# Optimization experiments

Measured on AMD Instinct MI355X. Metric: run time of the kernel, lower is better.

## Reference

```python
import jax, jax.numpy as jnp
import numpy as np

B, E, V, L = 16384, 16, 1_000_000, 50
DENSE, ONEHOT, MULTIHOT = 13, 26, 2
UNITS = [64, 12]
NN_IN = E * (ONEHOT + MULTIHOT) + DENSE  # 16*28+13 = 461
CONCAT_IN = 1 + E + UNITS[-1]            # 29


def setup_inputs() -> dict:
    key = jax.random.key(0)
    ks = jax.random.split(key, 12)
    s = 0.02  # glorot-ish init scale
    return {
        "dense": jax.random.normal(ks[0], (B, DENSE), jnp.float32),
        "onehot": jax.random.randint(ks[1], (B, ONEHOT), 0, V, jnp.int32),
        "multihot_ids": jax.random.randint(ks[2], (B, MULTIHOT, L), 0, V, jnp.int32),
        "multihot_mask": jnp.ones((B, MULTIHOT, L), jnp.float32),
        "fm_w": jax.random.normal(ks[3], (V, 1), jnp.float32) * s,
        "fm_emb": jax.random.normal(ks[4], (V, E), jnp.float32) * s,
        "nn_w0": jax.random.normal(ks[5], (NN_IN, UNITS[0]), jnp.float32) * s,
        "nn_b0": jnp.zeros((UNITS[0],), jnp.float32),
        "nn_w1": jax.random.normal(ks[6], (UNITS[0], UNITS[1]), jnp.float32) * s,
        "nn_b1": jnp.zeros((UNITS[1],), jnp.float32),
        "concat_w": jax.random.normal(ks[7], (CONCAT_IN, 1), jnp.float32) * s,
        "concat_b": jnp.zeros((1,), jnp.float32),
    }


def reference(dense, onehot, multihot_ids, multihot_mask, fm_w, fm_emb,
              nn_w0, nn_b0, nn_w1, nn_b1, concat_w, concat_b):
    # --- embedding lookups ---
    onehot_emb = fm_emb[onehot]                      # [B, 26, E]
    mh_emb = fm_emb[multihot_ids]                    # [B, 2, L, E]
    m = multihot_mask[..., None]                     # [B, 2, L, 1]
    # embedding_lookup_sparse(combiner='mean') over valid slots; empty rows -> 0 (tf.pad)
    denom = jnp.maximum(jnp.sum(m, axis=2), 1.0)     # [B, 2, 1]
    multihot_emb = jnp.sum(mh_emb * m, axis=2) / denom  # [B, 2, E]
    cat_emb = jnp.concatenate([onehot_emb, multihot_emb], axis=1)  # [B, 28, E]

    # --- FM 1st order: sum_i w_i (x_i = 1) ---
    fm_1st = jnp.sum(fm_w[onehot], axis=1)           # [B, 1]

    # --- FM 2nd order (keep_k_dims=True): 0.5*((sum v)^2 - sum v^2) ---
    s = jnp.sum(cat_emb, axis=1)                     # [B, E]
    fm_2nd = 0.5 * (s * s - jnp.sum(cat_emb * cat_emb, axis=1))  # [B, E]

    # --- deep part ---
    nn_inp = jnp.concatenate([cat_emb.reshape(-1, E * (ONEHOT + MULTIHOT)), dense], axis=1)
    h = jax.nn.relu(nn_inp @ nn_w0 + nn_b0)
    h = jax.nn.relu(h @ nn_w1 + nn_b1)               # [B, 12]

    concat_inp = jnp.concatenate([fm_1st, fm_2nd, h], axis=1)  # [B, 29]
    return jax.nn.sigmoid(concat_inp @ concat_w + concat_b)    # [B, 1]
```

## Files before the change

kernel.cpp:

```cpp
#include <hip/hip_runtime.h>
#include <hip/hip_bf16.h>

#define BATCH 16384
#define EDIM  16
#define NOH   26
#define LL    50
#define KIN   461
#define KPAD  480
#define KLDS  488
#define ROWS  32

using bf16x8 = __attribute__((ext_vector_type(8))) short;
using f32x4  = __attribute__((ext_vector_type(4))) float;

static __device__ __forceinline__ unsigned short f2bf(float f) {
    union { float f; unsigned int u; } v; v.f = f;
    unsigned int r = v.u + 0x7FFFu + ((v.u >> 16) & 1u);
    return (unsigned short)(r >> 16);
}
static __device__ __forceinline__ float bf2f(unsigned short u) {
    union { unsigned int u; float f; } v; v.u = ((unsigned int)u) << 16;
    return v.f;
}

__global__ __launch_bounds__(256) void prep(const float* __restrict__ w0,
                                            unsigned short* __restrict__ w0f) {
    int idx = blockIdx.x * 256 + threadIdx.x;
    if (idx < 30720) {
        int j    = idx & 7;
        int frag = idx >> 3;
        int lane = frag & 63;
        int tile = frag >> 6;
        int nt = tile / 15;
        int kt = tile - nt * 15;
        int k = kt * 32 + ((lane >> 4) << 3) + j;
        int n = (nt << 4) + (lane & 15);
        float v = (k < KIN) ? w0[k * 64 + n] : 0.f;
        w0f[idx] = f2bf(v);
    }
}

__global__ __launch_bounds__(512, 4) void fused(
    const float* __restrict__ dense,
    const int*   __restrict__ onehot,
    const int*   __restrict__ mh_ids,
    const float* __restrict__ mh_mask,
    const float* __restrict__ fm_w,
    const float* __restrict__ fm_emb,
    const unsigned short* __restrict__ w0f,
    const float* __restrict__ b0,
    const float* __restrict__ w1,
    const float* __restrict__ b1,
    const float* __restrict__ concat_w,
    const float* __restrict__ concat_b,
    float* __restrict__ out)
{
    __shared__ unsigned short As[ROWS * KLDS];
    __shared__ unsigned short h0s[ROWS][68];
    __shared__ float w1t[12 * 64];
    __shared__ float part_s[ROWS];
    __shared__ float b0s[64];
    __shared__ float b1s[12];
    __shared__ float cwh[12];

    const int t  = threadIdx.x;
    const int wv = t >> 6;
    const int l  = t & 63;
    const int s  = l >> 2;
    const int d  = l & 3;
    const int row0 = blockIdx.x << 5;

    for (int i = t; i < 768; i += 512) { int k = i / 12, j = i - k * 12; w1t[j * 64 + k] = w1[i]; }
    if (t < 64)               b0s[t] = b0[t];
    if (t >= 64 && t < 76)    b1s[t - 64] = b1[t - 64];
    if (t >= 96 && t < 108)   cwh[t - 96] = concat_w[17 + (t - 96)];

    for (int i = 0; i < 4; ++i) {
        const int r = (wv << 2) + i;
        const int b = row0 + r;

        const float v1 = (s < 10) ? 1.f : 0.f;
        int oid0 = onehot[b * NOH + s];
        int oid1 = (s < 10) ? onehot[b * NOH + 16 + s] : 0;

        int   mid[7]; float mmk[7];
        #pragma unroll
        for (int p = 0; p < 7; ++p) {
            int pi = p * 16 + s;
            bool valid = pi < 100;
            int f = (pi >= 50) ? 1 : 0;
            int ii = pi - f * 50;
            size_t off = ((size_t)b * 2 + f) * LL + ii;
            mid[p] = valid ? mh_ids[off]  : 0;
            mmk[p] = valid ? mh_mask[off] : 0.f;
        }

        float4 e0 = *(const float4*)(fm_emb + (size_t)oid0 * EDIM + d * 4);
        float4 e1 = *(const float4*)(fm_emb + (size_t)oid1 * EDIM + d * 4);
        float  wsa = fm_w[oid0];
        float  wsb = fm_w[oid1];
        float4 gm[7];
        #pragma unroll
        for (int p = 0; p < 7; ++p)
            gm[p] = *(const float4*)(fm_emb + (size_t)mid[p] * EDIM + d * 4);

        e1.x *= v1; e1.y *= v1; e1.z *= v1; e1.w *= v1;
        float wsum = (d == 0) ? (wsa + v1 * wsb) : 0.f;

        unsigned short* rowp = As + r * KLDS;
        {
            ushort4 u; u.x = f2bf(e0.x); u.y = f2bf(e0.y); u.z = f2bf(e0.z); u.w = f2bf(e0.w);
            *(ushort4*)(rowp + s * EDIM + d * 4) = u;
        }
        if (s < 10) {
            ushort4 u; u.x = f2bf(e1.x); u.y = f2bf(e1.y); u.z = f2bf(e1.z); u.w = f2bf(e1.w);
            *(ushort4*)(rowp + (16 + s) * EDIM + d * 4) = u;
        }

        float a0x=0,a0y=0,a0z=0,a0w=0, a1x=0,a1y=0,a1z=0,a1w=0, m0=0, m1=0;
        #pragma unroll
        for (int p = 0; p < 7; ++p) {
            int pi = p * 16 + s;
            float m = mmk[p];
            if (pi >= 50) { a1x += m*gm[p].x; a1y += m*gm[p].y; a1z += m*gm[p].z; a1w += m*gm[p].w; m1 += m; }
            else          { a0x += m*gm[p].x; a0y += m*gm[p].y; a0z += m*gm[p].z; a0w += m*gm[p].w; m0 += m; }
        }

        float ohx = e0.x + e1.x, ohy = e0.y + e1.y, ohz = e0.z + e1.z, ohw = e0.w + e1.w;
        float qx = e0.x*e0.x + e1.x*e1.x, qy = e0.y*e0.y + e1.y*e1.y;
        float qz = e0.z*e0.z + e1.z*e1.z, qw = e0.w*e0.w + e1.w*e1.w;

#define R4(v) { v += __shfl_xor(v, 4); v += __shfl_xor(v, 8); v += __shfl_xor(v, 16); v += __shfl_xor(v, 32); }
        R4(a0x) R4(a0y) R4(a0z) R4(a0w)
        R4(a1x) R4(a1y) R4(a1z) R4(a1w)
        R4(m0)  R4(m1)
        R4(ohx) R4(ohy) R4(ohz) R4(ohw)
        R4(qx)  R4(qy)  R4(qz)  R4(qw)
        R4(wsum)
#undef R4

        float inv0 = 1.f / fmaxf(m0, 1.f);
        float inv1 = 1.f / fmaxf(m1, 1.f);
        float h0x = a0x*inv0, h0y = a0y*inv0, h0z = a0z*inv0, h0w = a0w*inv0;
        float h1x = a1x*inv1, h1y = a1y*inv1, h1z = a1z*inv1, h1w = a1w*inv1;

        if (s == 0) {
            ushort4 u; u.x = f2bf(h0x); u.y = f2bf(h0y); u.z = f2bf(h0z); u.w = f2bf(h0w);
            *(ushort4*)(rowp + 26 * EDIM + d * 4) = u;
        }
        if (s == 1) {
            ushort4 u; u.x = f2bf(h1x); u.y = f2bf(h1y); u.z = f2bf(h1z); u.w = f2bf(h1w);
            *(ushort4*)(rowp + 27 * EDIM + d * 4) = u;
        }

        float sx = ohx + h0x + h1x, sy = ohy + h0y + h1y, sz = ohz + h0z + h1z, sw = ohw + h0w + h1w;
        float tx = qx + h0x*h0x + h1x*h1x, ty = qy + h0y*h0y + h1y*h1y;
        float tz = qz + h0z*h0z + h1z*h1z, tw = qw + h0w*h0w + h1w*h1w;
        float f2x = 0.5f * (sx*sx - tx), f2y = 0.5f * (sy*sy - ty);
        float f2z = 0.5f * (sz*sz - tz), f2w = 0.5f * (sw*sw - tw);

        float cw0 = concat_w[0];
        float c0 = concat_w[1 + d*4 + 0], c1 = concat_w[1 + d*4 + 1];
        float c2 = concat_w[1 + d*4 + 2], c3 = concat_w[1 + d*4 + 3];
        float part = f2x*c0 + f2y*c1 + f2z*c2 + f2w*c3 + wsum * cw0;
        part += __shfl_xor(part, 1);
        part += __shfl_xor(part, 2);
        if (l == 0) part_s[r] = part + concat_b[0];

        if (l < 32) {
            float v = (l < 13) ? dense[b * 13 + l] : 0.f;
            rowp[448 + l] = f2bf(v);
        }
    }
    __syncthreads();

    const int rt = wv >> 2, nt = wv & 3;
    const int c = l & 15, g = l >> 4;

    f32x4 acc = {0.f, 0.f, 0.f, 0.f};
    const unsigned short* ap = As + (rt * 16 + c) * KLDS + (g << 3);
    const unsigned short* bgp = w0f + ((size_t)(nt * 15) * 64 + l) * 8;

    #pragma unroll
    for (int kt = 0; kt < 15; ++kt) {
        bf16x8 a = *(const bf16x8*)(ap + kt * 32);
        bf16x8 bb = *(const bf16x8*)(bgp + (size_t)kt * 64 * 8);
        acc = __builtin_amdgcn_mfma_f32_16x16x32_bf16(a, bb, acc, 0, 0, 0);
    }

    #pragma unroll
    for (int reg = 0; reg < 4; ++reg)
        h0s[rt * 16 + g * 4 + reg][nt * 16 + c] = f2bf(fmaxf(acc[reg] + b0s[nt * 16 + c], 0.f));
    __syncthreads();

    if (wv < 2) {
        float s0 = b1s[g*3 + 0], s1 = b1s[g*3 + 1], s2 = b1s[g*3 + 2];
        const unsigned short* hrow = &h0s[wv * 16 + c][0];
        #pragma unroll
        for (int k8 = 0; k8 < 8; ++k8) {
            ushort4 ha = *(const ushort4*)(hrow + k8 * 8 + 0);
            ushort4 hb = *(const ushort4*)(hrow + k8 * 8 + 4);
            float h[8] = { bf2f(ha.x), bf2f(ha.y), bf2f(ha.z), bf2f(ha.w),
                           bf2f(hb.x), bf2f(hb.y), bf2f(hb.z), bf2f(hb.w) };
            #pragma unroll
            for (int j = 0; j < 8; ++j) {
                int k = k8 * 8 + j;
                s0 += h[j] * w1t[(g*3 + 0) * 64 + k];
                s1 += h[j] * w1t[(g*3 + 1) * 64 + k];
                s2 += h[j] * w1t[(g*3 + 2) * 64 + k];
            }
        }
        float hd = fmaxf(s0, 0.f)*cwh[g*3] + fmaxf(s1, 0.f)*cwh[g*3+1] + fmaxf(s2, 0.f)*cwh[g*3+2];
        hd += __shfl_xor(hd, 16);
        hd += __shfl_xor(hd, 32);
        if (g == 0) {
            int rr = row0 + wv * 16 + c;
            float x = part_s[wv * 16 + c] + hd;
            out[rr] = 1.f / (1.f + __expf(-x));
        }
    }
}

extern "C" void kernel_launch(void* const* d_in, const int* in_sizes, int n_in,
                              void* d_out, int out_size, void* d_ws, size_t ws_size,
                              hipStream_t stream) {
    const float* dense   = (const float*)d_in[0];
    const int*   onehot  = (const int*)  d_in[1];
    const int*   mh_ids  = (const int*)  d_in[2];
    const float* mh_mask = (const float*)d_in[3];
    const float* fm_w    = (const float*)d_in[4];
    const float* fm_emb  = (const float*)d_in[5];
    const float* w0      = (const float*)d_in[6];
    const float* b0      = (const float*)d_in[7];
    const float* w1      = (const float*)d_in[8];
    const float* b1      = (const float*)d_in[9];
    const float* cw      = (const float*)d_in[10];
    const float* cb      = (const float*)d_in[11];

    unsigned short* w0f = (unsigned short*)d_ws;

    hipLaunchKernelGGL(prep, dim3(120), dim3(256), 0, stream, w0, w0f);
    hipLaunchKernelGGL(fused, dim3(BATCH / ROWS), dim3(512), 0, stream,
                       dense, onehot, mh_ids, mh_mask, fm_w, fm_emb,
                       w0f, b0, w1, b1, cw, cb, (float*)d_out);
}
```

Baseline: 159.1 us.

## Overlap second-half embedding gather with first-half MFMA GEMM via warp specialization

The block's 32 rows are split into two 16-row halves. All 8 waves gather the first 16 rows. Then waves 0-3 run the MFMA layer-0 GEMM on that half while waves 4-7 gather the remaining 16 rows. The layer-1 tail for the first half overlaps with the second-half GEMM. The intent is to hide gather memory latency behind matrix work, at the cost of unbalanced per-wave work and an extra barrier stage.

```diff
diff --git a/kernel.cpp b/kernel.cpp
--- a/kernel.cpp
+++ b/kernel.cpp
@@ -75,10 +75,8 @@
     if (t >= 64 && t < 76)    b1s[t - 64] = b1[t - 64];
     if (t >= 96 && t < 108)   cwh[t - 96] = concat_w[17 + (t - 96)];
 
-    for (int i = 0; i < 4; ++i) {
-        const int r = (wv << 2) + i;
+    auto gather_row = [&](int r) {
         const int b = row0 + r;
-
         const float v1 = (s < 10) ? 1.f : 0.f;
         int oid0 = onehot[b * NOH + s];
         int oid1 = (s < 10) ? onehot[b * NOH + 16 + s] : 0;
@@ -171,54 +169,75 @@
             float v = (l < 13) ? dense[b * 13 + l] : 0.f;
             rowp[448 + l] = f2bf(v);
         }
-    }
-    __syncthreads();
-
-    const int rt = wv >> 2, nt = wv & 3;
+    };
+
     const int c = l & 15, g = l >> 4;
 
-    f32x4 acc = {0.f, 0.f, 0.f, 0.f};
-    const unsigned short* ap = As + (rt * 16 + c) * KLDS + (g << 3);
-    const unsigned short* bgp = w0f + ((size_t)(nt * 15) * 64 + l) * 8;
-
-    #pragma unroll
-    for (int kt = 0; kt < 15; ++kt) {
-        bf16x8 a = *(const bf16x8*)(ap + kt * 32);
-        bf16x8 bb = *(const bf16x8*)(bgp + (size_t)kt * 64 * 8);
-        acc = __builtin_amdgcn_mfma_f32_16x16x32_bf16(a, bb, acc, 0, 0, 0);
-    }
-
-    #pragma unroll
-    for (int reg = 0; reg < 4; ++reg)
-        h0s[rt * 16 + g * 4 + reg][nt * 16 + c] = f2bf(fmaxf(acc[reg] + b0s[nt * 16 + c], 0.f));
-    __syncthreads();
-
-    if (wv < 2) {
+    auto gemm_half = [&](int h, int nt) {
+        f32x4 acc = {0.f, 0.f, 0.f, 0.f};
+        const unsigned short* ap = As + (h * 16 + c) * KLDS + (g << 3);
+        const unsigned short* bgp = w0f + ((size_t)(nt * 15) * 64 + l) * 8;
+        #pragma unroll
+        for (int kt = 0; kt < 15; ++kt) {
+            bf16x8 a = *(const bf16x8*)(ap + kt * 32);
+            bf16x8 bb = *(const bf16x8*)(bgp + (size_t)kt * 64 * 8);
+            acc = __builtin_amdgcn_mfma_f32_16x16x32_bf16(a, bb, acc, 0, 0, 0);
+        }
+        #pragma unroll
+        for (int reg = 0; reg < 4; ++reg)
+            h0s[h * 16 + g * 4 + reg][nt * 16 + c] = f2bf(fmaxf(acc[reg] + b0s[nt * 16 + c], 0.f));
+    };
+
+    auto tail_half = [&](int h) {
         float s0 = b1s[g*3 + 0], s1 = b1s[g*3 + 1], s2 = b1s[g*3 + 2];
-        const unsigned short* hrow = &h0s[wv * 16 + c][0];
+        const unsigned short* hrow = &h0s[h * 16 + c][0];
         #pragma unroll
         for (int k8 = 0; k8 < 8; ++k8) {
             ushort4 ha = *(const ushort4*)(hrow + k8 * 8 + 0);
             ushort4 hb = *(const ushort4*)(hrow + k8 * 8 + 4);
-            float h[8] = { bf2f(ha.x), bf2f(ha.y), bf2f(ha.z), bf2f(ha.w),
-                           bf2f(hb.x), bf2f(hb.y), bf2f(hb.z), bf2f(hb.w) };
+            float hv[8] = { bf2f(ha.x), bf2f(ha.y), bf2f(ha.z), bf2f(ha.w),
+                            bf2f(hb.x), bf2f(hb.y), bf2f(hb.z), bf2f(hb.w) };
             #pragma unroll
             for (int j = 0; j < 8; ++j) {
                 int k = k8 * 8 + j;
-                s0 += h[j] * w1t[(g*3 + 0) * 64 + k];
-                s1 += h[j] * w1t[(g*3 + 1) * 64 + k];
-                s2 += h[j] * w1t[(g*3 + 2) * 64 + k];
+                s0 += hv[j] * w1t[(g*3 + 0) * 64 + k];
+                s1 += hv[j] * w1t[(g*3 + 1) * 64 + k];
+                s2 += hv[j] * w1t[(g*3 + 2) * 64 + k];
             }
         }
         float hd = fmaxf(s0, 0.f)*cwh[g*3] + fmaxf(s1, 0.f)*cwh[g*3+1] + fmaxf(s2, 0.f)*cwh[g*3+2];
         hd += __shfl_xor(hd, 16);
         hd += __shfl_xor(hd, 32);
         if (g == 0) {
-            int rr = row0 + wv * 16 + c;
-            float x = part_s[wv * 16 + c] + hd;
+            int rr = row0 + h * 16 + c;
+            float x = part_s[h * 16 + c] + hd;
             out[rr] = 1.f / (1.f + __expf(-x));
         }
+    };
+
+    gather_row(wv * 2 + 0);
+    gather_row(wv * 2 + 1);
+    __syncthreads();
+
+    if (wv < 4) {
+        gemm_half(0, wv);
+    } else {
+        const int base = 16 + (wv - 4) * 4;
+        gather_row(base + 0);
+        gather_row(base + 1);
+        gather_row(base + 2);
+        gather_row(base + 3);
     }
+    __syncthreads();
+
+    if (wv < 4) {
+        gemm_half(1, wv);
+    } else if (wv == 4) {
+        tail_half(0);
+    }
+    __syncthreads();
+
+    if (wv == 0) tail_half(1);
 }
 
 extern "C" void kernel_launch(void* const* d_in, const int* in_sizes, int n_in,
```

After: 159.1 us. About the same (-0.0%).
